# Performance work log

Hardware: AMD Instinct MI355X
Metric: run time of the kernel (lower is better)

## Reference

```python
import jax, jax.numpy as jnp
import numpy as np

PAD = 0
CONST_NO = 10000   # ids > CONST_NO are variables
N_PRED = 50
B, S, G = 8, 64, 8
F, R, BMAX = 200000, 200, 3
K_F, K_R = 64, 32  # max fact / rule children per state


def _is_var(x):
    return x > CONST_NO


def setup_inputs() -> dict:
    key = jax.random.key(0)
    ks = jax.random.split(key, 12)
    # facts: (pred, arg0, arg1), preds in [1, N_PRED], args are constants
    fp = jax.random.randint(ks[0], (F, 1), 1, N_PRED + 1, dtype=jnp.int32)
    fa = jax.random.randint(ks[1], (F, 2), 1, CONST_NO + 1, dtype=jnp.int32)
    facts = jnp.concatenate([fp, fa], axis=1)
    fact_scores = jax.random.uniform(ks[2], (F,), jnp.float32, 0.1, 1.0)
    # rule heads: p(V1, V2) with V1 = CONST_NO+1, V2 = CONST_NO+2
    hp = jax.random.randint(ks[3], (R, 1), 1, N_PRED + 1, dtype=jnp.int32)
    heads = jnp.concatenate([hp,
                             jnp.full((R, 1), CONST_NO + 1, jnp.int32),
                             jnp.full((R, 1), CONST_NO + 2, jnp.int32)], axis=1)
    # rule bodies: args are head vars or fresh constants
    bp = jax.random.randint(ks[4], (R, BMAX, 1), 1, N_PRED + 1, dtype=jnp.int32)
    choice = jax.random.randint(ks[5], (R, BMAX, 2), 0, 3, dtype=jnp.int32)
    consts = jax.random.randint(ks[6], (R, BMAX, 2), 1, CONST_NO + 1, dtype=jnp.int32)
    bargs = jnp.where(choice == 0, CONST_NO + 1,
                      jnp.where(choice == 1, CONST_NO + 2, consts)).astype(jnp.int32)
    bodies = jnp.concatenate([bp, bargs], axis=2)
    rule_lens = jax.random.randint(ks[7], (R,), 1, BMAX + 1, dtype=jnp.int32)
    rule_scores = jax.random.uniform(ks[8], (R,), jnp.float32, 0.1, 1.0)
    # proof goals [B,S,G,3]: args mix of constants and query vars CONST_NO+3/+4
    gp = jax.random.randint(ks[9], (B, S, G, 1), 1, N_PRED + 1, dtype=jnp.int32)
    vch = jax.random.randint(ks[10], (B, S, G, 2), 0, 4, dtype=jnp.int32)
    gc = jax.random.randint(ks[11], (B, S, G, 2), 1, CONST_NO + 1, dtype=jnp.int32)
    gargs = jnp.where(vch == 0, CONST_NO + 3,
                      jnp.where(vch == 1, CONST_NO + 4, gc)).astype(jnp.int32)
    goals = jnp.concatenate([gp, gargs], axis=3)
    # variable number of live goals per state (tail padded)
    pos = jnp.arange(G)
    keep = jax.random.randint(jax.random.fold_in(key, 99), (B, S, 1), 1, G + 1, dtype=jnp.int32)
    goals = jnp.where(pos[None, None, :, None] < keep[..., None], goals, PAD)
    state_scores = jax.random.uniform(jax.random.fold_in(key, 7), (B, S), jnp.float32, 0.1, 1.0)
    return dict(proof_goals=goals, state_scores=state_scores, facts=facts,
                fact_scores=fact_scores, heads=heads, bodies=bodies,
                rule_lens=rule_lens, rule_scores=rule_scores)


def reference(proof_goals, state_scores, facts, fact_scores, heads, bodies, rule_lens, rule_scores):
    # ---- 1. SELECT: query = goal slot 0, remaining goals mask slot 0 ----
    q = proof_goals[:, :, 0]                         # [B,S,3]
    active = q[..., 0] != PAD                        # [B,S]
    remaining = proof_goals.at[:, :, 0, :].set(PAD)  # [B,S,G,3]
    qp, qa0, qa1 = q[..., 0], q[..., 1], q[..., 2]

    # ---- 2. RESOLVE FACTS: unify query against fact table ----
    m = ((qp[..., None] == facts[:, 0])
         & (_is_var(qa0)[..., None] | (qa0[..., None] == facts[:, 1]))
         & (_is_var(qa1)[..., None] | (qa1[..., None] == facts[:, 2]))
         & active[..., None])                        # [B,S,F]
    fvals, fidx = jax.lax.top_k(m.astype(jnp.int32), K_F)
    fact_success = fvals > 0                         # [B,S,K_f]
    mf = facts[fidx]                                 # [B,S,K_f,3]
    # substitute query variables with matched fact constants in remaining goals
    v0 = qa0[:, :, None, None, None]
    v1 = qa1[:, :, None, None, None]
    b0 = mf[..., 1][..., None, None]
    b1 = mf[..., 2][..., None, None]
    rem = remaining[:, :, None]                      # [B,S,1,G,3]
    fg = jnp.where(_is_var(v0) & (rem == v0), b0, rem)
    fg = jnp.where(_is_var(v1) & (fg == v1), b1, fg)  # [B,S,K_f,G,3]
    fsc = jnp.where(fact_success, state_scores[:, :, None] * fact_scores[fidx], 0.0)

    # ---- 3. RESOLVE RULES: unify query against rule heads, append bodies ----
    mr = ((qp[..., None] == heads[:, 0])
          & (_is_var(heads[:, 1]) | _is_var(qa0)[..., None] | (qa0[..., None] == heads[:, 1]))
          & (_is_var(heads[:, 2]) | _is_var(qa1)[..., None] | (qa1[..., None] == heads[:, 2]))
          & active[..., None])                       # [B,S,R]
    rvals, ridx = jax.lax.top_k(mr.astype(jnp.int32), K_R)
    rule_success = rvals > 0                         # [B,S,K_r]
    mh = heads[ridx]                                 # [B,S,K_r,3]
    body = bodies[ridx]                              # [B,S,K_r,BMAX,3]
    h0 = mh[..., 1][..., None, None]
    h1 = mh[..., 2][..., None, None]
    qa0b = qa0[:, :, None, None, None]
    qa1b = qa1[:, :, None, None, None]
    body = jnp.where(_is_var(h0) & (body == h0), qa0b, body)
    body = jnp.where(_is_var(h1) & (body == h1), qa1b, body)
    bmask = jnp.arange(BMAX) < rule_lens[ridx][..., None]    # [B,S,K_r,BMAX]
    body = jnp.where(bmask[..., None], body, PAD)
    rem_rest = jnp.broadcast_to(remaining[:, :, None, 1:1 + (G - BMAX)], (B, S, K_R, G - BMAX, 3))
    rg = jnp.concatenate([body, rem_rest], axis=3)   # [B,S,K_r,G,3]
    rsc = jnp.where(rule_success, state_scores[:, :, None] * rule_scores[ridx], 0.0)

    # ---- 4. PACK: flatten SxK children, compact successful ones to S states ----
    K = K_F + K_R
    all_goals = jnp.concatenate([fg, rg], axis=2).reshape(B, S * K, G, 3)
    all_succ = jnp.concatenate([fact_success, rule_success], axis=2).reshape(B, S * K)
    all_sc = jnp.concatenate([fsc, rsc], axis=2).reshape(B, S * K)
    pvals, pidx = jax.lax.top_k(all_succ.astype(jnp.int32), S)
    new_succ = pvals > 0                             # [B,S]
    new_goals = jnp.take_along_axis(all_goals, pidx[..., None, None], axis=1)
    # ---- 5. POSTPROCESS: zero out failed / padded states ----
    new_goals = jnp.where(new_succ[..., None, None], new_goals, PAD)
    new_scores = jnp.where(new_succ, jnp.take_along_axis(all_sc, pidx, axis=1), 0.0)
    return new_goals, new_scores
```

## Files before the change

### kernel.cpp

```cpp
#include <hip/hip_runtime.h>

#define PAD 0
#define CONST_NO 10000
#define Bn 8
#define Sn 64
#define Gn 8
#define Fn 200000
#define Rn 200
#define BMAXn 3
#define KF 64
#define KR 32

#define NBLK 196
#define CHB  1024

#define WS_STRIDE   128
#define OFF_RES     0
#define OFF_STARTS  (Bn * Sn * WS_STRIDE)
#define OFF_COUNTS  (OFF_STARTS + 64)
#define OFF_BHIST   (OFF_COUNTS + 64)
#define OFF_SORT    78336

__device__ __forceinline__ bool isv(int x) { return x > CONST_NO; }

__global__ __launch_bounds__(256) void hist_kernel(
    const int* __restrict__ facts, int* __restrict__ ws)
{
    __shared__ int h[64];
    const int t = threadIdx.x;
    if (t < 64) h[t] = 0;
    __syncthreads();
    const int f0 = blockIdx.x * CHB + t * 4;
    if (f0 + 3 < Fn) {
        const int4* p4 = (const int4*)(facts + 3 * f0);
        int4 a = p4[0], b4 = p4[1], c4 = p4[2];
        atomicAdd(&h[a.x],  1);
        atomicAdd(&h[a.w],  1);
        atomicAdd(&h[b4.z], 1);
        atomicAdd(&h[c4.y], 1);
    } else {
        #pragma unroll
        for (int u = 0; u < 4; ++u)
            if (f0 + u < Fn) atomicAdd(&h[facts[3 * (f0 + u)]], 1);
    }
    __syncthreads();
    if (t < 64) ws[OFF_BHIST + blockIdx.x * 64 + t] = h[t];
}

__global__ __launch_bounds__(256) void scan_kernel(int* __restrict__ ws)
{
    __shared__ int part[4][64];
    __shared__ int qb[4][64];
    const int t = threadIdx.x;
    const int p = t & 63, q = t >> 6;
    const int b0 = q * 49, b1 = b0 + 49;

    int s = 0;
    for (int b = b0; b < b1; ++b) s += ws[OFF_BHIST + b * 64 + p];
    part[q][p] = s;
    __syncthreads();
    if (t < 64) {
        const int t0 = part[0][t], t1 = part[1][t], t2 = part[2][t], t3 = part[3][t];
        const int tot = t0 + t1 + t2 + t3;
        int incl = tot;
        #pragma unroll
        for (int off = 1; off < 64; off <<= 1) {
            int n = __shfl_up(incl, off, 64);
            if (t >= off) incl += n;
        }
        const int start = incl - tot;
        ws[OFF_STARTS + t] = start;
        ws[OFF_COUNTS + t] = tot;
        qb[0][t] = start;
        qb[1][t] = start + t0;
        qb[2][t] = start + t0 + t1;
        qb[3][t] = start + t0 + t1 + t2;
    }
    __syncthreads();
    int run = qb[q][p];
    for (int b = b0; b < b1; ++b) {
        const int v = ws[OFF_BHIST + b * 64 + p];
        ws[OFF_BHIST + b * 64 + p] = run;
        run += v;
    }
}

__global__ __launch_bounds__(256) void scatter_kernel(
    const int* __restrict__ facts, int* __restrict__ ws)
{
    __shared__ int predAll[CHB];
    __shared__ int coff[16][64];
    const int t = threadIdx.x;

    for (int k = t; k < 16 * 64; k += 256) ((int*)coff)[k] = 0;

    const int f0 = blockIdx.x * CHB + t * 4;
    int pv[4], a0v[4], a1v[4];
    int nvalid = 0;
    if (f0 + 3 < Fn) {
        const int4* p4 = (const int4*)(facts + 3 * f0);
        int4 a = p4[0], b4 = p4[1], c4 = p4[2];
        pv[0] = a.x;  a0v[0] = a.y;  a1v[0] = a.z;
        pv[1] = a.w;  a0v[1] = b4.x; a1v[1] = b4.y;
        pv[2] = b4.z; a0v[2] = b4.w; a1v[2] = c4.x;
        pv[3] = c4.y; a0v[3] = c4.z; a1v[3] = c4.w;
        nvalid = 4;
    } else {
        #pragma unroll
        for (int u = 0; u < 4; ++u) {
            pv[u] = -1; a0v[u] = 0; a1v[u] = 0;
            if (f0 + u < Fn) {
                pv[u]  = facts[3 * (f0 + u)];
                a0v[u] = facts[3 * (f0 + u) + 1];
                a1v[u] = facts[3 * (f0 + u) + 2];
                nvalid = u + 1;
            }
        }
    }
    const int c = t >> 4;
    #pragma unroll
    for (int u = 0; u < 4; ++u) {
        predAll[t * 4 + u] = pv[u];
        if (u < nvalid) atomicAdd(&coff[c][pv[u]], 1);
    }
    __syncthreads();
    if (t < 64) {
        int run = ws[OFF_BHIST + blockIdx.x * 64 + t];
        #pragma unroll
        for (int cc = 0; cc < 16; ++cc) {
            const int v = coff[cc][t];
            coff[cc][t] = run;
            run += v;
        }
    }
    __syncthreads();
    int4* sorted = (int4*)(ws + OFF_SORT);
    const int posb = (t & 15) * 4;
    #pragma unroll
    for (int u = 0; u < 4; ++u) {
        if (u < nvalid) {
            const int p = pv[u];
            int rank = 0;
            for (int j = 0; j < posb + u; ++j)
                rank += (predAll[c * 64 + j] == p);
            sorted[coff[c][p] + rank] = make_int4(a0v[u], a1v[u], f0 + u, 0);
        }
    }
}

__global__ __launch_bounds__(256) void match_kernel(
    const int* __restrict__ goals, const int* __restrict__ heads,
    int* __restrict__ ws)
{
    const int state = blockIdx.x;
    const int t = threadIdx.x;
    const int lane = t & 63, wv = t >> 6;
    __shared__ int wave_tot[4];

    const int* q = goals + state * (Gn * 3);
    const int qp = q[0], qa0 = q[1], qa1 = q[2];
    const bool active = (qp != PAD);
    const bool v0 = isv(qa0), v1 = isv(qa1);
    int* out = ws + OFF_RES + state * WS_STRIDE;

    const int st  = active ? ws[OFF_STARTS + qp] : 0;
    const int cnt = active ? ws[OFF_COUNTS + qp] : 0;
    const int4* S = (const int4*)(ws + OFF_SORT);

    if (v0 && v1) {
        const int n = (cnt < KF) ? cnt : KF;
        if (t < n) out[2 + t] = S[st + t].z;
        if (t == 0) out[0] = n;
    } else {
        int total = 0;
        for (int base = 0; base < cnt && total < KF; base += 512) {
            const int k0 = base + t * 2;
            unsigned mbits = 0;
            int i0 = 0, i1 = 0;
            if (k0 < cnt) {
                const int4 f = S[st + k0];
                i0 = f.z;
                if ((v0 || f.x == qa0) && (v1 || f.y == qa1)) mbits |= 1u;
            }
            if (k0 + 1 < cnt) {
                const int4 f = S[st + k0 + 1];
                i1 = f.z;
                if ((v0 || f.x == qa0) && (v1 || f.y == qa1)) mbits |= 2u;
            }
            const int c2 = __popc(mbits);

            int v = c2;
            #pragma unroll
            for (int off = 1; off < 64; off <<= 1) {
                int n = __shfl_up(v, off, 64);
                if (lane >= off) v += n;
            }
            if (lane == 63) wave_tot[wv] = v;
            __syncthreads();
            int excl = v - c2;
            #pragma unroll
            for (int w = 0; w < 4; ++w) if (w < wv) excl += wave_tot[w];
            const int ctot = wave_tot[0] + wave_tot[1] + wave_tot[2] + wave_tot[3];

            int pos = total + excl;
            if (mbits & 1u) { if (pos < KF) out[2 + pos] = i0; pos++; }
            if (mbits & 2u) { if (pos < KF) out[2 + pos] = i1; }
            total += ctot;
            __syncthreads();
        }
        if (t == 0) out[0] = (total < KF) ? total : KF;
    }

    int rcnt = 0;
    if (active && t < Rn) {
        const int h0 = heads[3 * t], h1 = heads[3 * t + 1], h2 = heads[3 * t + 2];
        if ((h0 == qp) && (isv(h1) || v0 || qa0 == h1)
                       && (isv(h2) || v1 || qa1 == h2))
            rcnt = 1;
    }
    __syncthreads();
    int v = rcnt;
    #pragma unroll
    for (int off = 1; off < 64; off <<= 1) {
        int n = __shfl_up(v, off, 64);
        if (lane >= off) v += n;
    }
    if (lane == 63) wave_tot[wv] = v;
    __syncthreads();
    int excl = v - rcnt;
    #pragma unroll
    for (int w = 0; w < 4; ++w) if (w < wv) excl += wave_tot[w];
    const int rtot = wave_tot[0] + wave_tot[1] + wave_tot[2] + wave_tot[3];
    if (rcnt && excl < KR) out[66 + excl] = t;
    if (t == 0) out[1] = (rtot < KR) ? rtot : KR;
}

__global__ __launch_bounds__(256) void select_kernel(
    const int* __restrict__ goals, const float* __restrict__ ss,
    const int* __restrict__ facts, const float* __restrict__ fsc,
    const int* __restrict__ heads, const int* __restrict__ bodies,
    const int* __restrict__ rlens, const float* __restrict__ rsc,
    const int* __restrict__ ws, float* __restrict__ outp)
{
    const int b = blockIdx.x, t = threadIdx.x;
    __shared__ int pref[Sn + 1];
    __shared__ int nf_s[Sn];

    if (t < Sn) {
        const int* w = ws + OFF_RES + (b * Sn + t) * WS_STRIDE;
        const int nf = w[0];
        nf_s[t] = nf;
        int val = nf + w[1];
        int incl = val;
        #pragma unroll
        for (int off = 1; off < 64; off <<= 1) {
            int n = __shfl_up(incl, off, 64);
            if (t >= off) incl += n;
        }
        pref[t + 1] = incl;
        if (t == 0) pref[0] = 0;
    }
    __syncthreads();
    const int total = pref[Sn];

    for (int item = t; item < Sn * Gn; item += 256) {
        const int i = item >> 3, g = item & 7;
        int trip[3] = {PAD, PAD, PAD};
        if (i < total) {
            int lo = 0, hi = Sn - 1;
            while (lo < hi) {
                const int mid = (lo + hi) >> 1;
                if (pref[mid + 1] <= i) lo = mid + 1; else hi = mid;
            }
            const int s = lo, j = i - pref[s];
            const int* w = ws + OFF_RES + (b * Sn + s) * WS_STRIDE;
            const int* q = goals + (b * Sn + s) * (Gn * 3);
            const int qa0 = q[1], qa1 = q[2];
            if (j < nf_s[s]) {
                const int fi = w[2 + j];
                const int f1 = facts[3 * fi + 1], f2 = facts[3 * fi + 2];
                if (g >= 1) {
                    #pragma unroll
                    for (int c = 0; c < 3; ++c) {
                        int x = q[g * 3 + c];
                        if (isv(qa0) && x == qa0) x = f1;
                        else if (isv(qa1) && x == qa1) x = f2;
                        trip[c] = x;
                    }
                }
            } else {
                const int ri = w[66 + (j - nf_s[s])];
                const int h1 = heads[3 * ri + 1], h2 = heads[3 * ri + 2];
                const int len = rlens[ri];
                if (g < BMAXn) {
                    if (g < len) {
                        #pragma unroll
                        for (int c = 0; c < 3; ++c) {
                            int x = bodies[(ri * BMAXn + g) * 3 + c];
                            if (isv(h1) && x == h1) x = qa0;
                            if (isv(h2) && x == h2) x = qa1;
                            trip[c] = x;
                        }
                    }
                } else {
                    trip[0] = q[(g - 2) * 3 + 0];
                    trip[1] = q[(g - 2) * 3 + 1];
                    trip[2] = q[(g - 2) * 3 + 2];
                }
            }
        }
        float* o = outp + ((b * Sn + i) * Gn + g) * 3;
        o[0] = (float)trip[0];
        o[1] = (float)trip[1];
        o[2] = (float)trip[2];
    }

    if (t < Sn) {
        const int i = t;
        float sc = 0.f;
        if (i < total) {
            int lo = 0, hi = Sn - 1;
            while (lo < hi) {
                const int mid = (lo + hi) >> 1;
                if (pref[mid + 1] <= i) lo = mid + 1; else hi = mid;
            }
            const int s = lo, j = i - pref[s];
            const int* w = ws + OFF_RES + (b * Sn + s) * WS_STRIDE;
            const float stt = ss[b * Sn + s];
            if (j < nf_s[s]) sc = stt * fsc[w[2 + j]];
            else             sc = stt * rsc[w[66 + (j - nf_s[s])]];
        }
        outp[Bn * Sn * Gn * 3 + b * Sn + t] = sc;
    }
}

extern "C" void kernel_launch(void* const* d_in, const int* in_sizes, int n_in,
                              void* d_out, int out_size, void* d_ws, size_t ws_size,
                              hipStream_t stream) {
    const int*   goals  = (const int*)  d_in[0];
    const float* ss     = (const float*)d_in[1];
    const int*   facts  = (const int*)  d_in[2];
    const float* fsc    = (const float*)d_in[3];
    const int*   heads  = (const int*)  d_in[4];
    const int*   bodies = (const int*)  d_in[5];
    const int*   rlens  = (const int*)  d_in[6];
    const float* rsc    = (const float*)d_in[7];
    int*   ws   = (int*)d_ws;
    float* outp = (float*)d_out;

    hist_kernel   <<<NBLK,   256, 0, stream>>>(facts, ws);
    scan_kernel   <<<1,      256, 0, stream>>>(ws);
    scatter_kernel<<<NBLK,   256, 0, stream>>>(facts, ws);
    match_kernel  <<<Bn * Sn,256, 0, stream>>>(goals, heads, ws);
    select_kernel <<<Bn,     256, 0, stream>>>(goals, ss, facts, fsc, heads, bodies,
                                               rlens, rsc, ws, outp);
}
```

Baseline: 103.0 us.

## Fuse match and select kernels using last-block-done atomic counter per batch

Merges the per-state match kernel and the per-batch select kernel into one launch. Each block increments a per-batch atomic counter after writing its results, and the last block of each batch runs the select logic. Counters are zeroed in the hist kernel. This removes one kernel launch and its inter-kernel gap, at the cost of threadfences, atomics, and a serialized tail where select runs inside one late block per batch.

Measured after the change: 111.0 us. +7.8%, slower.

```diff
diff --git a/kernel.cpp b/kernel.cpp
--- a/kernel.cpp
+++ b/kernel.cpp
@@ -18,7 +18,8 @@
 #define OFF_RES     0
 #define OFF_STARTS  (Bn * Sn * WS_STRIDE)
 #define OFF_COUNTS  (OFF_STARTS + 64)
-#define OFF_BHIST   (OFF_COUNTS + 64)
+#define OFF_CTR     (OFF_COUNTS + 64)
+#define OFF_BHIST   (OFF_CTR + 16)
 #define OFF_SORT    78336
 
 __device__ __forceinline__ bool isv(int x) { return x > CONST_NO; }
@@ -28,6 +29,7 @@
 {
     __shared__ int h[64];
     const int t = threadIdx.x;
+    if (blockIdx.x == 0 && t < 16) ws[OFF_CTR + t] = 0;
     if (t < 64) h[t] = 0;
     __syncthreads();
     const int f0 = blockIdx.x * CHB + t * 4;
@@ -148,104 +150,15 @@
     }
 }
 
-__global__ __launch_bounds__(256) void match_kernel(
-    const int* __restrict__ goals, const int* __restrict__ heads,
-    int* __restrict__ ws)
-{
-    const int state = blockIdx.x;
-    const int t = threadIdx.x;
-    const int lane = t & 63, wv = t >> 6;
-    __shared__ int wave_tot[4];
-
-    const int* q = goals + state * (Gn * 3);
-    const int qp = q[0], qa0 = q[1], qa1 = q[2];
-    const bool active = (qp != PAD);
-    const bool v0 = isv(qa0), v1 = isv(qa1);
-    int* out = ws + OFF_RES + state * WS_STRIDE;
-
-    const int st  = active ? ws[OFF_STARTS + qp] : 0;
-    const int cnt = active ? ws[OFF_COUNTS + qp] : 0;
-    const int4* S = (const int4*)(ws + OFF_SORT);
-
-    if (v0 && v1) {
-        const int n = (cnt < KF) ? cnt : KF;
-        if (t < n) out[2 + t] = S[st + t].z;
-        if (t == 0) out[0] = n;
-    } else {
-        int total = 0;
-        for (int base = 0; base < cnt && total < KF; base += 512) {
-            const int k0 = base + t * 2;
-            unsigned mbits = 0;
-            int i0 = 0, i1 = 0;
-            if (k0 < cnt) {
-                const int4 f = S[st + k0];
-                i0 = f.z;
-                if ((v0 || f.x == qa0) && (v1 || f.y == qa1)) mbits |= 1u;
-            }
-            if (k0 + 1 < cnt) {
-                const int4 f = S[st + k0 + 1];
-                i1 = f.z;
-                if ((v0 || f.x == qa0) && (v1 || f.y == qa1)) mbits |= 2u;
-            }
-            const int c2 = __popc(mbits);
-
-            int v = c2;
-            #pragma unroll
-            for (int off = 1; off < 64; off <<= 1) {
-                int n = __shfl_up(v, off, 64);
-                if (lane >= off) v += n;
-            }
-            if (lane == 63) wave_tot[wv] = v;
-            __syncthreads();
-            int excl = v - c2;
-            #pragma unroll
-            for (int w = 0; w < 4; ++w) if (w < wv) excl += wave_tot[w];
-            const int ctot = wave_tot[0] + wave_tot[1] + wave_tot[2] + wave_tot[3];
-
-            int pos = total + excl;
-            if (mbits & 1u) { if (pos < KF) out[2 + pos] = i0; pos++; }
-            if (mbits & 2u) { if (pos < KF) out[2 + pos] = i1; }
-            total += ctot;
-            __syncthreads();
-        }
-        if (t == 0) out[0] = (total < KF) ? total : KF;
-    }
-
-    int rcnt = 0;
-    if (active && t < Rn) {
-        const int h0 = heads[3 * t], h1 = heads[3 * t + 1], h2 = heads[3 * t + 2];
-        if ((h0 == qp) && (isv(h1) || v0 || qa0 == h1)
-                       && (isv(h2) || v1 || qa1 == h2))
-            rcnt = 1;
-    }
-    __syncthreads();
-    int v = rcnt;
-    #pragma unroll
-    for (int off = 1; off < 64; off <<= 1) {
-        int n = __shfl_up(v, off, 64);
-        if (lane >= off) v += n;
-    }
-    if (lane == 63) wave_tot[wv] = v;
-    __syncthreads();
-    int excl = v - rcnt;
-    #pragma unroll
-    for (int w = 0; w < 4; ++w) if (w < wv) excl += wave_tot[w];
-    const int rtot = wave_tot[0] + wave_tot[1] + wave_tot[2] + wave_tot[3];
-    if (rcnt && excl < KR) out[66 + excl] = t;
-    if (t == 0) out[1] = (rtot < KR) ? rtot : KR;
-}
-
-__global__ __launch_bounds__(256) void select_kernel(
+__device__ void do_select(
+    int b, int t,
     const int* __restrict__ goals, const float* __restrict__ ss,
     const int* __restrict__ facts, const float* __restrict__ fsc,
     const int* __restrict__ heads, const int* __restrict__ bodies,
     const int* __restrict__ rlens, const float* __restrict__ rsc,
-    const int* __restrict__ ws, float* __restrict__ outp)
-{
-    const int b = blockIdx.x, t = threadIdx.x;
-    __shared__ int pref[Sn + 1];
-    __shared__ int nf_s[Sn];
-
+    const int* __restrict__ ws, float* __restrict__ outp,
+    int* pref, int* nf_s)
+{
     if (t < Sn) {
         const int* w = ws + OFF_RES + (b * Sn + t) * WS_STRIDE;
         const int nf = w[0];
@@ -334,6 +247,112 @@
     }
 }
 
+__global__ __launch_bounds__(256) void match_select_kernel(
+    const int* __restrict__ goals, const float* __restrict__ ss,
+    const int* __restrict__ facts, const float* __restrict__ fsc,
+    const int* __restrict__ heads, const int* __restrict__ bodies,
+    const int* __restrict__ rlens, const float* __restrict__ rsc,
+    int* __restrict__ ws, float* __restrict__ outp)
+{
+    const int state = blockIdx.x;
+    const int t = threadIdx.x;
+    const int lane = t & 63, wv = t >> 6;
+    __shared__ int wave_tot[4];
+    __shared__ int sel_flag;
+    __shared__ int pref[Sn + 1];
+    __shared__ int nf_s[Sn];
+
+    const int* q = goals + state * (Gn * 3);
+    const int qp = q[0], qa0 = q[1], qa1 = q[2];
+    const bool active = (qp != PAD);
+    const bool v0 = isv(qa0), v1 = isv(qa1);
+    int* out = ws + OFF_RES + state * WS_STRIDE;
+
+    const int st  = active ? ws[OFF_STARTS + qp] : 0;
+    const int cnt = active ? ws[OFF_COUNTS + qp] : 0;
+    const int4* S = (const int4*)(ws + OFF_SORT);
+
+    if (v0 && v1) {
+        const int n = (cnt < KF) ? cnt : KF;
+        if (t < n) out[2 + t] = S[st + t].z;
+        if (t == 0) out[0] = n;
+    } else {
+        int total = 0;
+        for (int base = 0; base < cnt && total < KF; base += 512) {
+            const int k0 = base + t * 2;
+            unsigned mbits = 0;
+            int i0 = 0, i1 = 0;
+            if (k0 < cnt) {
+                const int4 f = S[st + k0];
+                i0 = f.z;
+                if ((v0 || f.x == qa0) && (v1 || f.y == qa1)) mbits |= 1u;
+            }
+            if (k0 + 1 < cnt) {
+                const int4 f = S[st + k0 + 1];
+                i1 = f.z;
+                if ((v0 || f.x == qa0) && (v1 || f.y == qa1)) mbits |= 2u;
+            }
+            const int c2 = __popc(mbits);
+
+            int v = c2;
+            #pragma unroll
+            for (int off = 1; off < 64; off <<= 1) {
+                int n = __shfl_up(v, off, 64);
+                if (lane >= off) v += n;
+            }
+            if (lane == 63) wave_tot[wv] = v;
+            __syncthreads();
+            int excl = v - c2;
+            #pragma unroll
+            for (int w = 0; w < 4; ++w) if (w < wv) excl += wave_tot[w];
+            const int ctot = wave_tot[0] + wave_tot[1] + wave_tot[2] + wave_tot[3];
+
+            int pos = total + excl;
+            if (mbits & 1u) { if (pos < KF) out[2 + pos] = i0; pos++; }
+            if (mbits & 2u) { if (pos < KF) out[2 + pos] = i1; }
+            total += ctot;
+            __syncthreads();
+        }
+        if (t == 0) out[0] = (total < KF) ? total : KF;
+    }
+
+    int rcnt = 0;
+    if (active && t < Rn) {
+        const int h0 = heads[3 * t], h1 = heads[3 * t + 1], h2 = heads[3 * t + 2];
+        if ((h0 == qp) && (isv(h1) || v0 || qa0 == h1)
+                       && (isv(h2) || v1 || qa1 == h2))
+            rcnt = 1;
+    }
+    __syncthreads();
+    int v = rcnt;
+    #pragma unroll
+    for (int off = 1; off < 64; off <<= 1) {
+        int n = __shfl_up(v, off, 64);
+        if (lane >= off) v += n;
+    }
+    if (lane == 63) wave_tot[wv] = v;
+    __syncthreads();
+    int excl = v - rcnt;
+    #pragma unroll
+    for (int w = 0; w < 4; ++w) if (w < wv) excl += wave_tot[w];
+    const int rtot = wave_tot[0] + wave_tot[1] + wave_tot[2] + wave_tot[3];
+    if (rcnt && excl < KR) out[66 + excl] = t;
+    if (t == 0) out[1] = (rtot < KR) ? rtot : KR;
+
+    const int b = state >> 6;
+    __syncthreads();
+    if (t == 0) {
+        __threadfence();
+        const int old = atomicAdd(ws + OFF_CTR + b, 1);
+        sel_flag = (old == Sn - 1);
+    }
+    __syncthreads();
+    if (!sel_flag) return;
+    __threadfence();
+    do_select(b, t, goals, ss, facts, fsc, heads, bodies, rlens, rsc,
+              ws, outp, pref, nf_s);
+}
+
 extern "C" void kernel_launch(void* const* d_in, const int* in_sizes, int n_in,
                               void* d_out, int out_size, void* d_ws, size_t ws_size,
                               hipStream_t stream) {
@@ -348,10 +367,9 @@
     int*   ws   = (int*)d_ws;
     float* outp = (float*)d_out;
 
-    hist_kernel   <<<NBLK,   256, 0, stream>>>(facts, ws);
-    scan_kernel   <<<1,      256, 0, stream>>>(ws);
-    scatter_kernel<<<NBLK,   256, 0, stream>>>(facts, ws);
-    match_kernel  <<<Bn * Sn,256, 0, stream>>>(goals, heads, ws);
-    select_kernel <<<Bn,     256, 0, stream>>>(goals, ss, facts, fsc, heads, bodies,
-                                               rlens, rsc, ws, outp);
-}
+    hist_kernel        <<<NBLK,    256, 0, stream>>>(facts, ws);
+    scan_kernel        <<<1,       256, 0, stream>>>(ws);
+    scatter_kernel     <<<NBLK,    256, 0, stream>>>(facts, ws);
+    match_select_kernel<<<Bn * Sn, 256, 0, stream>>>(goals, ss, facts, fsc, heads,
+                                                     bodies, rlens, rsc, ws, outp);
+}
```

## Fold prefix scan into scatter, widen match loads, split select across blocks

Applied to the files above, without the earlier changes.

Removes the single-block scan kernel: every scatter block now recomputes the global per-predicate totals and its own block prefix from the histogram, and block 0 writes the starts and counts. The match loop now has each thread examine four sorted facts per iteration instead of two, halving the iterations and barriers per chunk. Select now launches eight blocks per batch, each writing one eighth of the output states, which raises parallelism. The cost is redundant histogram reads in every scatter block and a repeated prefix computation in every select block.

New measurement: 95.33 us. -7.4%, faster.

```diff
diff --git a/kernel.cpp b/kernel.cpp
--- a/kernel.cpp
+++ b/kernel.cpp
@@ -47,54 +47,32 @@
     if (t < 64) ws[OFF_BHIST + blockIdx.x * 64 + t] = h[t];
 }
 
-__global__ __launch_bounds__(256) void scan_kernel(int* __restrict__ ws)
-{
-    __shared__ int part[4][64];
-    __shared__ int qb[4][64];
-    const int t = threadIdx.x;
-    const int p = t & 63, q = t >> 6;
-    const int b0 = q * 49, b1 = b0 + 49;
-
-    int s = 0;
-    for (int b = b0; b < b1; ++b) s += ws[OFF_BHIST + b * 64 + p];
-    part[q][p] = s;
-    __syncthreads();
-    if (t < 64) {
-        const int t0 = part[0][t], t1 = part[1][t], t2 = part[2][t], t3 = part[3][t];
-        const int tot = t0 + t1 + t2 + t3;
-        int incl = tot;
-        #pragma unroll
-        for (int off = 1; off < 64; off <<= 1) {
-            int n = __shfl_up(incl, off, 64);
-            if (t >= off) incl += n;
-        }
-        const int start = incl - tot;
-        ws[OFF_STARTS + t] = start;
-        ws[OFF_COUNTS + t] = tot;
-        qb[0][t] = start;
-        qb[1][t] = start + t0;
-        qb[2][t] = start + t0 + t1;
-        qb[3][t] = start + t0 + t1 + t2;
-    }
-    __syncthreads();
-    int run = qb[q][p];
-    for (int b = b0; b < b1; ++b) {
-        const int v = ws[OFF_BHIST + b * 64 + p];
-        ws[OFF_BHIST + b * 64 + p] = run;
-        run += v;
-    }
-}
-
 __global__ __launch_bounds__(256) void scatter_kernel(
     const int* __restrict__ facts, int* __restrict__ ws)
 {
     __shared__ int predAll[CHB];
     __shared__ int coff[16][64];
+    __shared__ int partAll[4][64];
+    __shared__ int partPre[4][64];
     const int t = threadIdx.x;
+    const int lane = t & 63, wv = t >> 6;
+    const int B = blockIdx.x;
 
     for (int k = t; k < 16 * 64; k += 256) ((int*)coff)[k] = 0;
 
-    const int f0 = blockIdx.x * CHB + t * 4;
+    {
+        const int b0 = wv * 49, b1 = b0 + 49;
+        int sA = 0, sP = 0;
+        for (int b = b0; b < b1; ++b) {
+            const int v = ws[OFF_BHIST + b * 64 + lane];
+            sA += v;
+            if (b < B) sP += v;
+        }
+        partAll[wv][lane] = sA;
+        partPre[wv][lane] = sP;
+    }
+
+    const int f0 = B * CHB + t * 4;
     int pv[4], a0v[4], a1v[4];
     int nvalid = 0;
     if (f0 + 3 < Fn) {
@@ -117,6 +95,9 @@
             }
         }
     }
+
+    __syncthreads();
+
     const int c = t >> 4;
     #pragma unroll
     for (int u = 0; u < 4; ++u) {
@@ -124,8 +105,22 @@
         if (u < nvalid) atomicAdd(&coff[c][pv[u]], 1);
     }
     __syncthreads();
+
     if (t < 64) {
-        int run = ws[OFF_BHIST + blockIdx.x * 64 + t];
+        const int tot = partAll[0][t] + partAll[1][t] + partAll[2][t] + partAll[3][t];
+        const int pre = partPre[0][t] + partPre[1][t] + partPre[2][t] + partPre[3][t];
+        int incl = tot;
+        #pragma unroll
+        for (int off = 1; off < 64; off <<= 1) {
+            int n = __shfl_up(incl, off, 64);
+            if (t >= off) incl += n;
+        }
+        const int start = incl - tot;
+        if (B == 0) {
+            ws[OFF_STARTS + t] = start;
+            ws[OFF_COUNTS + t] = tot;
+        }
+        int run = start + pre;
         #pragma unroll
         for (int cc = 0; cc < 16; ++cc) {
             const int v = coff[cc][t];
@@ -134,6 +129,7 @@
         }
     }
     __syncthreads();
+
     int4* sorted = (int4*)(ws + OFF_SORT);
     const int posb = (t & 15) * 4;
     #pragma unroll
@@ -173,23 +169,22 @@
         if (t == 0) out[0] = n;
     } else {
         int total = 0;
-        for (int base = 0; base < cnt && total < KF; base += 512) {
-            const int k0 = base + t * 2;
+        for (int base = 0; base < cnt && total < KF; base += 1024) {
+            const int k0 = base + t * 4;
             unsigned mbits = 0;
-            int i0 = 0, i1 = 0;
-            if (k0 < cnt) {
-                const int4 f = S[st + k0];
-                i0 = f.z;
-                if ((v0 || f.x == qa0) && (v1 || f.y == qa1)) mbits |= 1u;
-            }
-            if (k0 + 1 < cnt) {
-                const int4 f = S[st + k0 + 1];
-                i1 = f.z;
-                if ((v0 || f.x == qa0) && (v1 || f.y == qa1)) mbits |= 2u;
-            }
-            const int c2 = __popc(mbits);
-
-            int v = c2;
+            int idxv[4];
+            #pragma unroll
+            for (int u = 0; u < 4; ++u) {
+                idxv[u] = 0;
+                if (k0 + u < cnt) {
+                    const int4 f = S[st + k0 + u];
+                    idxv[u] = f.z;
+                    if ((v0 || f.x == qa0) && (v1 || f.y == qa1)) mbits |= (1u << u);
+                }
+            }
+            const int c4 = __popc(mbits);
+
+            int v = c4;
             #pragma unroll
             for (int off = 1; off < 64; off <<= 1) {
                 int n = __shfl_up(v, off, 64);
@@ -197,14 +192,19 @@
             }
             if (lane == 63) wave_tot[wv] = v;
             __syncthreads();
-            int excl = v - c2;
+            int excl = v - c4;
             #pragma unroll
             for (int w = 0; w < 4; ++w) if (w < wv) excl += wave_tot[w];
             const int ctot = wave_tot[0] + wave_tot[1] + wave_tot[2] + wave_tot[3];
 
             int pos = total + excl;
-            if (mbits & 1u) { if (pos < KF) out[2 + pos] = i0; pos++; }
-            if (mbits & 2u) { if (pos < KF) out[2 + pos] = i1; }
+            #pragma unroll
+            for (int u = 0; u < 4; ++u) {
+                if (mbits & (1u << u)) {
+                    if (pos < KF) out[2 + pos] = idxv[u];
+                    pos++;
+                }
+            }
             total += ctot;
             __syncthreads();
         }
@@ -242,7 +242,9 @@
     const int* __restrict__ rlens, const float* __restrict__ rsc,
     const int* __restrict__ ws, float* __restrict__ outp)
 {
-    const int b = blockIdx.x, t = threadIdx.x;
+    const int b = blockIdx.x >> 3;
+    const int k = blockIdx.x & 7;
+    const int t = threadIdx.x;
     __shared__ int pref[Sn + 1];
     __shared__ int nf_s[Sn];
 
@@ -263,8 +265,8 @@
     __syncthreads();
     const int total = pref[Sn];
 
-    for (int item = t; item < Sn * Gn; item += 256) {
-        const int i = item >> 3, g = item & 7;
+    if (t < 64) {
+        const int i = k * 8 + (t >> 3), g = t & 7;
         int trip[3] = {PAD, PAD, PAD};
         if (i < total) {
             int lo = 0, hi = Sn - 1;
@@ -313,10 +315,8 @@
         o[0] = (float)trip[0];
         o[1] = (float)trip[1];
         o[2] = (float)trip[2];
-    }
-
-    if (t < Sn) {
-        const int i = t;
+    } else if (t >= 128 && t < 136) {
+        const int i = k * 8 + (t - 128);
         float sc = 0.f;
         if (i < total) {
             int lo = 0, hi = Sn - 1;
@@ -330,7 +330,7 @@
             if (j < nf_s[s]) sc = stt * fsc[w[2 + j]];
             else             sc = stt * rsc[w[66 + (j - nf_s[s])]];
         }
-        outp[Bn * Sn * Gn * 3 + b * Sn + t] = sc;
+        outp[Bn * Sn * Gn * 3 + b * Sn + i] = sc;
     }
 }
 
@@ -348,10 +348,9 @@
     int*   ws   = (int*)d_ws;
     float* outp = (float*)d_out;
 
-    hist_kernel   <<<NBLK,   256, 0, stream>>>(facts, ws);
-    scan_kernel   <<<1,      256, 0, stream>>>(ws);
-    scatter_kernel<<<NBLK,   256, 0, stream>>>(facts, ws);
-    match_kernel  <<<Bn * Sn,256, 0, stream>>>(goals, heads, ws);
-    select_kernel <<<Bn,     256, 0, stream>>>(goals, ss, facts, fsc, heads, bodies,
-                                               rlens, rsc, ws, outp);
-}
+    hist_kernel   <<<NBLK,    256, 0, stream>>>(facts, ws);
+    scatter_kernel<<<NBLK,    256, 0, stream>>>(facts, ws);
+    match_kernel  <<<Bn * Sn, 256, 0, stream>>>(goals, heads, ws);
+    select_kernel <<<Bn * 8,  256, 0, stream>>>(goals, ss, facts, fsc, heads,
+                                                bodies, rlens, rsc, ws, outp);
+}
```
